# Optimization experiments

Measured on AMD Instinct MI355X. Metric: run time of the kernel, lower is better.

## Reference

```python
import jax, jax.numpy as jnp
import numpy as np

B, X, Y, Z = 8, 32, 32, 32
Dx = Dy = Dz = 128
K = 256   # h_dim * k, k=1
H = 2     # h_out
EPS = 1e-5


def _wn(V, g):
    # weight_norm with dim=None: W = g * V / ||V||_F (g scalar)
    return (g / jnp.linalg.norm(V)) * V


def setup_inputs() -> dict:
    key = jax.random.key(0)
    ks = jax.random.split(key, 8)
    x = jax.random.normal(ks[0], (B, X, Dx), jnp.float32)
    y = jax.random.normal(ks[1], (B, Y, Dy), jnp.float32)
    z = jax.random.normal(ks[2], (B, Z, Dz), jnp.float32)
    Vx = jax.random.normal(ks[3], (K, Dx), jnp.float32) * 0.05
    Vy = jax.random.normal(ks[4], (K, Dy), jnp.float32) * 0.05
    Vz = jax.random.normal(ks[5], (K, Dz), jnp.float32) * 0.05
    Vh = jax.random.normal(ks[6], (H, K), jnp.float32) * 0.05
    return {
        "x": x, "y": y, "z": z,
        "Vx": Vx, "gx": jnp.linalg.norm(Vx), "bx": jnp.zeros((K,), jnp.float32),
        "Vy": Vy, "gy": jnp.linalg.norm(Vy), "by": jnp.zeros((K,), jnp.float32),
        "Vz": Vz, "gz": jnp.linalg.norm(Vz), "bz": jnp.zeros((K,), jnp.float32),
        "Vh": Vh, "gh": jnp.linalg.norm(Vh), "bh": jnp.zeros((H,), jnp.float32),
        "gamma": jnp.ones((K,), jnp.float32), "beta": jnp.zeros((K,), jnp.float32),
    }


def reference(x, y, z, Vx, gx, bx, Vy, gy, by, Vz, gz, bz, Vh, gh, bh, gamma, beta):
    relu = jax.nn.relu
    _x = relu(x @ _wn(Vx, gx).T + bx)  # [B,X,K]
    _y = relu(y @ _wn(Vy, gy).T + by)  # [B,Y,K]
    _z = relu(z @ _wn(Vz, gz).T + bz)  # [B,Z,K]
    # trilinear outer product: [B,X,Y,Z,K] (memory-explosive intermediate)
    xyz = jnp.einsum('bxk,byk,bzk->bxyzk', _x, _y, _z)
    att = jnp.einsum('bxyzk,hk->bhxyz', xyz, _wn(Vh, gh)) + bh[None, :, None, None, None]
    # softmax over flattened X*Y*Z per head
    att = jax.nn.softmax(att.reshape(B, H, -1), axis=-1).reshape(B, H, X, Y, Z)
    # attention pooling, summed over all h_out heads (equals the torch loop)
    att_sum = att.sum(axis=1)  # [B,X,Y,Z]
    logits = jnp.einsum('bxk,byk,bzk,bxyz->bk', _x, _y, _z, att_sum)  # [B,K]
    # BatchNorm1d (training-mode batch stats, biased variance)
    mean = logits.mean(axis=0)
    var = logits.var(axis=0)
    out = (logits - mean) / jnp.sqrt(var + EPS) * gamma + beta
    return (out, att)
```

## Files before the change

### kernel.cpp

```cpp
#include <hip/hip_runtime.h>
#include <math.h>

#define BB 8
#define DD 128
#define KK 256
#define XYZ 32768
#define EPSV 1e-5f

#define WS_X     0
#define WS_Y     65536
#define WS_Z     131072
#define WS_RAW   196608
#define WS_SM    (WS_RAW + 524288)
#define WS_PART  (WS_SM + 1024)

__global__ void __launch_bounds__(256)
tan_proj_kernel(const float* x, const float* y, const float* z,
                const float* Vx, const float* Vy, const float* Vz,
                const float* gx, const float* gy, const float* gz,
                const float* bx, const float* by, const float* bz,
                float* ws) {
    __shared__ float lin[4 * DD];
    __shared__ float wred[4];
    int bid = blockIdx.x;
    int t = threadIdx.x;
    int which = bid >> 6;
    int rgrp = bid & 63;
    int r0 = rgrp * 4;
    const float *in, *V, *g, *bias;
    float* outp;
    if (which == 0)      { in = x; V = Vx; g = gx; bias = bx; outp = ws + WS_X; }
    else if (which == 1) { in = y; V = Vy; g = gy; bias = by; outp = ws + WS_Y; }
    else                 { in = z; V = Vz; g = gz; bias = bz; outp = ws + WS_Z; }
    {
        int f0 = t, f1 = t + 256;
        lin[f0] = in[(r0 + (f0 >> 7)) * DD + (f0 & 127)];
        lin[f1] = in[(r0 + (f1 >> 7)) * DD + (f1 & 127)];
    }
    __syncthreads();
    const float4* v4 = (const float4*)(V + t * DD);
    const float4* l4 = (const float4*)lin;
    float a0 = 0.f, a1 = 0.f, a2 = 0.f, a3 = 0.f, ssp = 0.f;
#pragma unroll 8
    for (int d4 = 0; d4 < DD / 4; ++d4) {
        float4 a = v4[d4];
        ssp += a.x * a.x + a.y * a.y + a.z * a.z + a.w * a.w;
        float4 b0 = l4[d4];
        float4 b1 = l4[32 + d4];
        float4 b2 = l4[64 + d4];
        float4 b3 = l4[96 + d4];
        a0 += a.x * b0.x + a.y * b0.y + a.z * b0.z + a.w * b0.w;
        a1 += a.x * b1.x + a.y * b1.y + a.z * b1.z + a.w * b1.w;
        a2 += a.x * b2.x + a.y * b2.y + a.z * b2.z + a.w * b2.w;
        a3 += a.x * b3.x + a.y * b3.y + a.z * b3.z + a.w * b3.w;
    }
#pragma unroll
    for (int o = 32; o > 0; o >>= 1) ssp += __shfl_xor(ssp, o);
    if ((t & 63) == 0) wred[t >> 6] = ssp;
    __syncthreads();
    float ss = wred[0] + wred[1] + wred[2] + wred[3];
    float scale = g[0] * rsqrtf(ss);
    float bv = bias[t];
    outp[(r0 + 0) * KK + t] = fmaxf(a0 * scale + bv, 0.f);
    outp[(r0 + 1) * KK + t] = fmaxf(a1 * scale + bv, 0.f);
    outp[(r0 + 2) * KK + t] = fmaxf(a2 * scale + bv, 0.f);
    outp[(r0 + 3) * KK + t] = fmaxf(a3 * scale + bv, 0.f);
}

__global__ void __launch_bounds__(512)
tan_score_kernel(const float* __restrict__ Vh, const float* __restrict__ gh,
                 const float* __restrict__ bh, float* __restrict__ ws) {
    __shared__ float ys[32 * 256];
    __shared__ float zs[32 * 256];
    __shared__ float shh;
    __shared__ float smred[8][4];
    int t = threadIdx.x;
    int bb = blockIdx.x >> 5;
    int xx = blockIdx.x & 31;
    const float* _xb = ws + WS_X + (bb * 32 + xx) * KK;
    const float* _yb = ws + WS_Y + bb * 8192;
    const float* _zb = ws + WS_Z + bb * 8192;

    if (t < 64) {
        float4 h1 = *(const float4*)(Vh + t * 8);
        float4 h2 = *(const float4*)(Vh + t * 8 + 4);
        float hs = h1.x * h1.x + h1.y * h1.y + h1.z * h1.z + h1.w * h1.w
                 + h2.x * h2.x + h2.y * h2.y + h2.z * h2.z + h2.w * h2.w;
#pragma unroll
        for (int o = 32; o > 0; o >>= 1) hs += __shfl_xor(hs, o);
        if (t == 0) shh = hs;
    }

#pragma unroll
    for (int i = 0; i < 4; ++i) {
        int flat = i * 2048 + t * 4;
        int row = flat >> 8;
        int k = flat & 255;
        int gsw = (((k >> 2) ^ (row & 7)) << 2);
        *(float4*)(ys + row * 256 + gsw) = *(const float4*)(_yb + flat);
        *(float4*)(zs + row * 256 + gsw) = *(const float4*)(_zb + flat);
    }
    __syncthreads();
    float sh = gh[0] * rsqrtf(shh);

    int ty = t >> 4;
    int tz = t & 15;
    int z0 = tz, z1 = tz + 16;
    int ysw = (ty & 7);
    int zsw = (tz & 7);

    float s00 = 0.f, s01 = 0.f, s10 = 0.f, s11 = 0.f;

#pragma unroll 4
    for (int kc = 0; kc < 256; kc += 4) {
        int g = kc >> 2;
        float4 xv  = *(const float4*)(_xb + kc);
        float4 vh0 = *(const float4*)(Vh + kc);
        float4 vh1 = *(const float4*)(Vh + KK + kc);
        float4 ya = *(const float4*)(ys + ty * 256 + ((g ^ ysw) << 2));
        float4 za = *(const float4*)(zs + z0 * 256 + ((g ^ zsw) << 2));
        float4 zb = *(const float4*)(zs + z1 * 256 + ((g ^ zsw) << 2));
#define TAN_STEP(c) { \
        float xs = sh * xv.c; \
        float w0 = xs * vh0.c, w1 = xs * vh1.c; \
        float t0 = w0 * ya.c, t1 = w1 * ya.c; \
        s00 = fmaf(t0, za.c, s00); s01 = fmaf(t0, zb.c, s01); \
        s10 = fmaf(t1, za.c, s10); s11 = fmaf(t1, zb.c, s11); }
        TAN_STEP(x) TAN_STEP(y) TAN_STEP(z) TAN_STEP(w)
#undef TAN_STEP
    }

    float b0 = bh[0], b1 = bh[1];
    s00 += b0; s01 += b0;
    s10 += b1; s11 += b1;
    float* r0 = ws + WS_RAW + (bb * 2 + 0) * XYZ + xx * 1024;
    float* r1 = r0 + XYZ;
    r0[ty * 32 + z0] = s00;  r0[ty * 32 + z1] = s01;
    r1[ty * 32 + z0] = s10;  r1[ty * 32 + z1] = s11;

    float m0 = fmaxf(s00, s01);
    float l0 = __expf(s00 - m0) + __expf(s01 - m0);
    float m1 = fmaxf(s10, s11);
    float l1 = __expf(s10 - m1) + __expf(s11 - m1);
#pragma unroll
    for (int o = 1; o < 64; o <<= 1) {
        float mo = __shfl_xor(m0, o), lo = __shfl_xor(l0, o);
        float nm = fmaxf(m0, mo);
        l0 = l0 * __expf(m0 - nm) + lo * __expf(mo - nm); m0 = nm;
        mo = __shfl_xor(m1, o); lo = __shfl_xor(l1, o);
        nm = fmaxf(m1, mo);
        l1 = l1 * __expf(m1 - nm) + lo * __expf(mo - nm); m1 = nm;
    }
    if ((t & 63) == 0) {
        int w = t >> 6;
        smred[w][0] = m0; smred[w][1] = l0;
        smred[w][2] = m1; smred[w][3] = l1;
    }
    __syncthreads();
    if (t == 0) {
        float M0 = smred[0][0], L0 = smred[0][1];
        float M1 = smred[0][2], L1 = smred[0][3];
#pragma unroll
        for (int w = 1; w < 8; ++w) {
            float nm = fmaxf(M0, smred[w][0]);
            L0 = L0 * __expf(M0 - nm) + smred[w][1] * __expf(smred[w][0] - nm);
            M0 = nm;
            nm = fmaxf(M1, smred[w][2]);
            L1 = L1 * __expf(M1 - nm) + smred[w][3] * __expf(smred[w][2] - nm);
            M1 = nm;
        }
        float* sm = ws + WS_SM + (bb * 32 + xx) * 4;
        sm[0] = M0; sm[1] = L0; sm[2] = M1; sm[3] = L1;
    }
}

__global__ void __launch_bounds__(512)
tan_logits_kernel(float* __restrict__ ws, float* __restrict__ out) {
    __shared__ float as4[1024];
    __shared__ float cons[4];
    __shared__ float pacc[512];
    int b = blockIdx.x >> 5;
    int x = blockIdx.x & 31;
    int t = threadIdx.x;
    int k = t & 255;
    int half = t >> 8;
    const float* _zb = ws + WS_Z + b * 8192;
    float zreg[32];
#pragma unroll
    for (int zi = 0; zi < 32; ++zi) zreg[zi] = _zb[zi * 256 + k];

    if (t < 64) {
        const float* sm = ws + WS_SM + (b * 32 + (t & 31)) * 4;
        float4 p = *(const float4*)sm;
        float m0 = p.x, l0 = p.y, m1 = p.z, l1 = p.w;
#pragma unroll
        for (int o = 1; o < 32; o <<= 1) {
            float mo = __shfl_xor(m0, o), lo = __shfl_xor(l0, o);
            float nm = fmaxf(m0, mo);
            l0 = l0 * __expf(m0 - nm) + lo * __expf(mo - nm); m0 = nm;
            mo = __shfl_xor(m1, o); lo = __shfl_xor(l1, o);
            nm = fmaxf(m1, mo);
            l1 = l1 * __expf(m1 - nm) + lo * __expf(mo - nm); m1 = nm;
        }
        if (t == 0) {
            cons[0] = m0; cons[1] = 1.f / l0;
            cons[2] = m1; cons[3] = 1.f / l1;
        }
    }
    __syncthreads();
    float M0 = cons[0], inv0 = cons[1], M1 = cons[2], inv1 = cons[3];
    const float* r0 = ws + WS_RAW + (b * 2) * XYZ + x * 1024;
    const float* r1 = r0 + XYZ;
    float* o0 = out + BB * KK + (b * 2) * XYZ + x * 1024;
    float* o1 = o0 + XYZ;
#pragma unroll
    for (int i = t; i < 1024; i += 512) {
        float a0 = __expf(r0[i] - M0) * inv0;
        float a1 = __expf(r1[i] - M1) * inv1;
        o0[i] = a0; o1[i] = a1;
        as4[i] = a0 + a1;
    }
    __syncthreads();

    const float* _yb = ws + WS_Y + b * 8192;
    float acc = 0.f;
    int y0 = half * 16;
#pragma unroll 4
    for (int yi = 0; yi < 16; ++yi) {
        int yy = y0 + yi;
        float s = 0.f;
        const float4* ar = (const float4*)(as4 + yy * 32);
#pragma unroll
        for (int j = 0; j < 8; ++j) {
            float4 a = ar[j];
            s += a.x * zreg[j * 4] + a.y * zreg[j * 4 + 1]
               + a.z * zreg[j * 4 + 2] + a.w * zreg[j * 4 + 3];
        }
        acc = fmaf(_yb[yy * 256 + k], s, acc);
    }
    pacc[t] = acc;
    __syncthreads();
    if (t < 256) {
        float xv = ws[WS_X + (b * 32 + x) * 256 + t];
        ws[WS_PART + (b * 32 + x) * 256 + t] = xv * (pacc[t] + pacc[t + 256]);
    }
}

__global__ void __launch_bounds__(1024)
tan_bn_kernel(const float* ws, const float* gamma, const float* beta, float* out) {
    __shared__ float red[8192];
    int t = threadIdx.x;
    int tg = t >> 8;
    int k = t & 255;
    const float* part = ws + WS_PART;
    float lg[BB];
#pragma unroll
    for (int b = 0; b < BB; ++b) {
        float s = 0.f;
#pragma unroll
        for (int xi = 0; xi < 8; ++xi)
            s += part[(b * 32 + tg * 8 + xi) * 256 + k];
        red[tg * 2048 + b * 256 + k] = s;
    }
    __syncthreads();
    if (tg == 0) {
#pragma unroll
        for (int b = 0; b < BB; ++b)
            lg[b] = red[b * 256 + k] + red[2048 + b * 256 + k]
                  + red[4096 + b * 256 + k] + red[6144 + b * 256 + k];
        float mean = 0.f;
#pragma unroll
        for (int b = 0; b < BB; ++b) mean += lg[b];
        mean *= 0.125f;
        float var = 0.f;
#pragma unroll
        for (int b = 0; b < BB; ++b) { float d = lg[b] - mean; var += d * d; }
        var *= 0.125f;
        float inv = rsqrtf(var + EPSV);
        float gm = gamma[k], bt = beta[k];
#pragma unroll
        for (int b = 0; b < BB; ++b)
            out[b * 256 + k] = (lg[b] - mean) * inv * gm + bt;
    }
}

extern "C" void kernel_launch(void* const* d_in, const int* in_sizes, int n_in,
                              void* d_out, int out_size, void* d_ws, size_t ws_size,
                              hipStream_t stream) {
    (void)in_sizes; (void)n_in; (void)out_size; (void)ws_size;
    const float* x     = (const float*)d_in[0];
    const float* y     = (const float*)d_in[1];
    const float* z     = (const float*)d_in[2];
    const float* Vx    = (const float*)d_in[3];
    const float* gx    = (const float*)d_in[4];
    const float* bx    = (const float*)d_in[5];
    const float* Vy    = (const float*)d_in[6];
    const float* gy    = (const float*)d_in[7];
    const float* by    = (const float*)d_in[8];
    const float* Vz    = (const float*)d_in[9];
    const float* gz    = (const float*)d_in[10];
    const float* bz    = (const float*)d_in[11];
    const float* Vh    = (const float*)d_in[12];
    const float* gh    = (const float*)d_in[13];
    const float* bh    = (const float*)d_in[14];
    const float* gamma = (const float*)d_in[15];
    const float* beta  = (const float*)d_in[16];
    float* ws  = (float*)d_ws;
    float* out = (float*)d_out;

    tan_proj_kernel<<<192, 256, 0, stream>>>(x, y, z, Vx, Vy, Vz,
                                             gx, gy, gz, bx, by, bz, ws);
    tan_score_kernel<<<256, 512, 0, stream>>>(Vh, gh, bh, ws);
    tan_logits_kernel<<<256, 512, 0, stream>>>(ws, out);
    tan_bn_kernel<<<1, 1024, 0, stream>>>(ws, gamma, beta, out);
}
```

Baseline: 119.7 us.

## Fuse projection into score kernel, recomputing y/z projections per block

Removes the separate projection kernel and computes the y and z projections (32 rows × 256 outputs each) directly inside every score block, writing them straight into shared memory. The x row projection is computed per block as well. Only the xx==0 block stores y/z projections to the workspace for the later logits kernel. This saves one kernel launch and a global round trip, at the cost of repeating the y/z projection work across all 32 blocks per batch and adding register pressure from 32 accumulators per thread.

```diff
diff --git a/kernel.cpp b/kernel.cpp
--- a/kernel.cpp
+++ b/kernel.cpp
@@ -14,72 +14,33 @@
 #define WS_SM    (WS_RAW + 524288)
 #define WS_PART  (WS_SM + 1024)
 
-__global__ void __launch_bounds__(256)
-tan_proj_kernel(const float* x, const float* y, const float* z,
-                const float* Vx, const float* Vy, const float* Vz,
-                const float* gx, const float* gy, const float* gz,
-                const float* bx, const float* by, const float* bz,
-                float* ws) {
-    __shared__ float lin[4 * DD];
-    __shared__ float wred[4];
-    int bid = blockIdx.x;
-    int t = threadIdx.x;
-    int which = bid >> 6;
-    int rgrp = bid & 63;
-    int r0 = rgrp * 4;
-    const float *in, *V, *g, *bias;
-    float* outp;
-    if (which == 0)      { in = x; V = Vx; g = gx; bias = bx; outp = ws + WS_X; }
-    else if (which == 1) { in = y; V = Vy; g = gy; bias = by; outp = ws + WS_Y; }
-    else                 { in = z; V = Vz; g = gz; bias = bz; outp = ws + WS_Z; }
-    {
-        int f0 = t, f1 = t + 256;
-        lin[f0] = in[(r0 + (f0 >> 7)) * DD + (f0 & 127)];
-        lin[f1] = in[(r0 + (f1 >> 7)) * DD + (f1 & 127)];
-    }
-    __syncthreads();
-    const float4* v4 = (const float4*)(V + t * DD);
-    const float4* l4 = (const float4*)lin;
-    float a0 = 0.f, a1 = 0.f, a2 = 0.f, a3 = 0.f, ssp = 0.f;
-#pragma unroll 8
-    for (int d4 = 0; d4 < DD / 4; ++d4) {
-        float4 a = v4[d4];
-        ssp += a.x * a.x + a.y * a.y + a.z * a.z + a.w * a.w;
-        float4 b0 = l4[d4];
-        float4 b1 = l4[32 + d4];
-        float4 b2 = l4[64 + d4];
-        float4 b3 = l4[96 + d4];
-        a0 += a.x * b0.x + a.y * b0.y + a.z * b0.z + a.w * b0.w;
-        a1 += a.x * b1.x + a.y * b1.y + a.z * b1.z + a.w * b1.w;
-        a2 += a.x * b2.x + a.y * b2.y + a.z * b2.z + a.w * b2.w;
-        a3 += a.x * b3.x + a.y * b3.y + a.z * b3.z + a.w * b3.w;
-    }
-#pragma unroll
-    for (int o = 32; o > 0; o >>= 1) ssp += __shfl_xor(ssp, o);
-    if ((t & 63) == 0) wred[t >> 6] = ssp;
-    __syncthreads();
-    float ss = wred[0] + wred[1] + wred[2] + wred[3];
-    float scale = g[0] * rsqrtf(ss);
-    float bv = bias[t];
-    outp[(r0 + 0) * KK + t] = fmaxf(a0 * scale + bv, 0.f);
-    outp[(r0 + 1) * KK + t] = fmaxf(a1 * scale + bv, 0.f);
-    outp[(r0 + 2) * KK + t] = fmaxf(a2 * scale + bv, 0.f);
-    outp[(r0 + 3) * KK + t] = fmaxf(a3 * scale + bv, 0.f);
-}
+#define SWZ(row, kk) ((row) * 256 + (((((kk) >> 2) ^ ((row) & 7)) << 2) | ((kk) & 3)))
+
+#define NRM4(s, a) { s += (a).x*(a).x + (a).y*(a).y + (a).z*(a).z + (a).w*(a).w; }
+#define DOT4(s, a, b) { s = fmaf((a).x,(b).x, fmaf((a).y,(b).y, fmaf((a).z,(b).z, fmaf((a).w,(b).w,(s))))); }
 
 __global__ void __launch_bounds__(512)
-tan_score_kernel(const float* __restrict__ Vh, const float* __restrict__ gh,
-                 const float* __restrict__ bh, float* __restrict__ ws) {
+tan_projscore_kernel(const float* __restrict__ x, const float* __restrict__ y,
+                     const float* __restrict__ z,
+                     const float* __restrict__ Vx, const float* __restrict__ Vy,
+                     const float* __restrict__ Vz,
+                     const float* __restrict__ gx, const float* __restrict__ gy,
+                     const float* __restrict__ gz,
+                     const float* __restrict__ bx, const float* __restrict__ by,
+                     const float* __restrict__ bz,
+                     const float* __restrict__ Vh, const float* __restrict__ gh,
+                     const float* __restrict__ bh, float* __restrict__ ws) {
     __shared__ float ys[32 * 256];
     __shared__ float zs[32 * 256];
+    __shared__ float xsh[256];
+    __shared__ float nred[16];
+    __shared__ float smred[8][4];
     __shared__ float shh;
-    __shared__ float smred[8][4];
     int t = threadIdx.x;
     int bb = blockIdx.x >> 5;
     int xx = blockIdx.x & 31;
-    const float* _xb = ws + WS_X + (bb * 32 + xx) * KK;
-    const float* _yb = ws + WS_Y + bb * 8192;
-    const float* _zb = ws + WS_Z + bb * 8192;
+    int k = t & 255;
+    int half = __builtin_amdgcn_readfirstlane(t >> 8);
 
     if (t < 64) {
         float4 h1 = *(const float4*)(Vh + t * 8);
@@ -91,16 +52,87 @@
         if (t == 0) shh = hs;
     }
 
-#pragma unroll
-    for (int i = 0; i < 4; ++i) {
-        int flat = i * 2048 + t * 4;
-        int row = flat >> 8;
-        int k = flat & 255;
-        int gsw = (((k >> 2) ^ (row & 7)) << 2);
-        *(float4*)(ys + row * 256 + gsw) = *(const float4*)(_yb + flat);
-        *(float4*)(zs + row * 256 + gsw) = *(const float4*)(_zb + flat);
-    }
-    __syncthreads();
+    const float* inp  = half ? (z + bb * 32 * DD) : (y + bb * 32 * DD);
+    const float* V    = half ? Vz : Vy;
+    const float* bias = half ? bz : by;
+    const float* gg   = half ? gz : gy;
+    const float4* v4  = (const float4*)(V + k * DD);
+
+    float acc[32];
+#pragma unroll
+    for (int r = 0; r < 32; ++r) acc[r] = 0.f;
+    float ssp = 0.f;
+
+#pragma unroll
+    for (int dg = 0; dg < 8; ++dg) {
+        float4 a0 = v4[dg * 4 + 0];
+        float4 a1 = v4[dg * 4 + 1];
+        float4 a2 = v4[dg * 4 + 2];
+        float4 a3 = v4[dg * 4 + 3];
+        NRM4(ssp, a0) NRM4(ssp, a1) NRM4(ssp, a2) NRM4(ssp, a3)
+#pragma unroll
+        for (int r = 0; r < 32; ++r) {
+            const float4* bp = (const float4*)(inp + r * DD + dg * 16);
+            float4 b0 = bp[0], b1 = bp[1], b2 = bp[2], b3 = bp[3];
+            float s = acc[r];
+            DOT4(s, a0, b0) DOT4(s, a1, b1) DOT4(s, a2, b2) DOT4(s, a3, b3)
+            acc[r] = s;
+        }
+    }
+
+    float xacc = 0.f, ssxp = 0.f;
+    if (half == 0) {
+        const float4* vx4 = (const float4*)(Vx + k * DD);
+        const float* xr = x + (bb * 32 + xx) * DD;
+#pragma unroll
+        for (int dg = 0; dg < 8; ++dg) {
+            float4 a0 = vx4[dg * 4 + 0];
+            float4 a1 = vx4[dg * 4 + 1];
+            float4 a2 = vx4[dg * 4 + 2];
+            float4 a3 = vx4[dg * 4 + 3];
+            NRM4(ssxp, a0) NRM4(ssxp, a1) NRM4(ssxp, a2) NRM4(ssxp, a3)
+            const float4* bp = (const float4*)(xr + dg * 16);
+            float4 b0 = bp[0], b1 = bp[1], b2 = bp[2], b3 = bp[3];
+            DOT4(xacc, a0, b0) DOT4(xacc, a1, b1) DOT4(xacc, a2, b2) DOT4(xacc, a3, b3)
+        }
+    }
+
+    {
+        float s1 = ssp, s2 = ssxp;
+#pragma unroll
+        for (int o = 32; o > 0; o >>= 1) {
+            s1 += __shfl_xor(s1, o);
+            s2 += __shfl_xor(s2, o);
+        }
+        int w = t >> 6;
+        if ((t & 63) == 0) { nred[w * 2] = s1; nred[w * 2 + 1] = s2; }
+    }
+    __syncthreads();
+    float ssY = nred[0] + nred[2] + nred[4] + nred[6];
+    float ssX = nred[1] + nred[3] + nred[5] + nred[7];
+    float ssZ = nred[8] + nred[10] + nred[12] + nred[14];
+
+    {
+        float scl = gg[0] * rsqrtf(half ? ssZ : ssY);
+        float bv = bias[k];
+        float* lbuf = half ? zs : ys;
+        float* gbuf = ws + (half ? WS_Z : WS_Y) + bb * 8192;
+        bool store_g = (xx == 0);
+#pragma unroll
+        for (int r = 0; r < 32; ++r) {
+            float v = fmaxf(acc[r] * scl + bv, 0.f);
+            lbuf[SWZ(r, k)] = v;
+            if (store_g) gbuf[r * 256 + k] = v;
+        }
+        if (half == 0) {
+            float xscl = gx[0] * rsqrtf(ssX);
+            float xv = fmaxf(xacc * xscl + bx[k], 0.f);
+            xsh[k] = xv;
+            ws[WS_X + (bb * 32 + xx) * 256 + k] = xv;
+        }
+    }
+    __syncthreads();
+
     float sh = gh[0] * rsqrtf(shh);
 
     int ty = t >> 4;
@@ -114,7 +146,7 @@
 #pragma unroll 4
     for (int kc = 0; kc < 256; kc += 4) {
         int g = kc >> 2;
-        float4 xv  = *(const float4*)(_xb + kc);
+        float4 xv  = *(const float4*)(xsh + kc);
         float4 vh0 = *(const float4*)(Vh + kc);
         float4 vh1 = *(const float4*)(Vh + KK + kc);
         float4 ya = *(const float4*)(ys + ty * 256 + ((g ^ ysw) << 2));
@@ -308,9 +340,9 @@
     float* ws  = (float*)d_ws;
     float* out = (float*)d_out;
 
-    tan_proj_kernel<<<192, 256, 0, stream>>>(x, y, z, Vx, Vy, Vz,
-                                             gx, gy, gz, bx, by, bz, ws);
-    tan_score_kernel<<<256, 512, 0, stream>>>(Vh, gh, bh, ws);
+    tan_projscore_kernel<<<256, 512, 0, stream>>>(x, y, z, Vx, Vy, Vz,
+                                                  gx, gy, gz, bx, by, bz,
+                                                  Vh, gh, bh, ws);
     tan_logits_kernel<<<256, 512, 0, stream>>>(ws, out);
     tan_bn_kernel<<<1, 1024, 0, stream>>>(ws, gamma, beta, out);
 }
```

Result: slower. 242.3 us (+102.4%).
